# Optimization experiments

Measured on AMD Instinct MI355X. Metric: run time of the kernel, lower is better.

Reference implementation:

```python
import jax, jax.numpy as jnp
import numpy as np

NUM_STEPS = 8
THRESHOLD = 0.5


def _glorot(key, shape):
    fan_in = shape[0]
    return jax.random.normal(key, shape, dtype=jnp.float32) / np.sqrt(fan_in).astype(np.float32)


def setup_inputs() -> dict:
    key = jax.random.key(0)
    ks = jax.random.split(key, 24)
    B, APM = 2048, 32           # molecules, atoms per molecule
    N = B * APM                 # 65536 nodes
    E = N * 4                   # 262144 directed edges
    NF, EF, NH, EH, MA = 64, 16, 128, 128, 256
    inp = {}
    inp['mol_a_reprs'] = jax.random.normal(ks[0], (B, MA), dtype=jnp.float32)
    inp['node_features'] = jax.random.normal(ks[1], (N, NF), dtype=jnp.float32)
    inp['edge_features'] = jax.random.normal(ks[2], (E, EF), dtype=jnp.float32)
    inp['node_hidden0'] = jnp.zeros((N, NH), dtype=jnp.float32)
    inp['edge_hidden0'] = jnp.zeros((E, EH), dtype=jnp.float32)
    inp['edges'] = jax.random.randint(ks[3], (2, E), 0, N, dtype=jnp.int32)
    inp['batch_indices'] = jnp.repeat(jnp.arange(B, dtype=jnp.int32), APM)  # sorted, in-range
    # MPN weights (no bias)
    inp['W1'] = _glorot(ks[4], (NF, EH))   # src node features -> edge hidden
    inp['W2'] = _glorot(ks[5], (EF, EH))   # edge features -> edge hidden
    inp['W3'] = _glorot(ks[6], (NH, EH))   # src node hidden -> edge hidden
    inp['U1'] = _glorot(ks[7], (NF, NH))   # node features -> node hidden
    inp['U2'] = _glorot(ks[8], (EH, NH))   # aggregated edge hidden -> node hidden
    # pick-atom MLP: (MA+NH)->256->128->64->1
    inp['M1w'] = _glorot(ks[9], (MA + NH, 256)); inp['M1b'] = jnp.zeros((256,), jnp.float32)
    inp['M2w'] = _glorot(ks[10], (256, 128));    inp['M2b'] = jnp.zeros((128,), jnp.float32)
    inp['M3w'] = _glorot(ks[11], (128, 64));     inp['M3b'] = jnp.zeros((64,), jnp.float32)
    inp['M4w'] = _glorot(ks[12], (64, 1));       inp['M4b'] = jnp.zeros((1,), jnp.float32)
    return inp


def _mpn(node_features, edge_features, node_h, edge_h, src, dst, W1, W2, W3, U1, U2):
    N = node_features.shape[0]
    W1x_src = node_features[src] @ W1          # [E, EH], loop-invariant
    W2e = edge_features @ W2                   # [E, EH], loop-invariant
    U1x = node_features @ U1                   # [N, NH], loop-invariant
    for _ in range(NUM_STEPS):
        agg = jax.ops.segment_sum(edge_h, dst, num_segments=N)   # [N, EH]
        node_h = jax.nn.relu(U1x + agg @ U2)                     # [N, NH]
        edge_h = jax.nn.relu(W1x_src + W2e + node_h[src] @ W3)   # [E, EH]
    return node_h


def reference(mol_a_reprs, node_features, edge_features, node_hidden0, edge_hidden0,
              edges, batch_indices, W1, W2, W3, U1, U2,
              M1w, M1b, M2w, M2b, M3w, M3b, M4w, M4b):
    src, dst = edges[0], edges[1]
    node_h = _mpn(node_features, edge_features, node_hidden0, edge_hidden0,
                  src, dst, W1, W2, W3, U1, U2)
    b_atom_mol_a = mol_a_reprs[batch_indices]                    # index_select gather [N, MA]
    x = jnp.concatenate([node_h, b_atom_mol_a], axis=1)          # [N, NH+MA]
    x = jax.nn.relu(x @ M1w + M1b)
    x = jax.nn.relu(x @ M2w + M2b)
    x = jax.nn.relu(x @ M3w + M3b)
    p = jax.nn.sigmoid(x @ M4w + M4b)                            # [N, 1]
    return p >= THRESHOLD
```

## Files before the change

### kernel.cpp

```cpp
#include <hip/hip_runtime.h>
#include <cstddef>

#define NF 64
#define EF 16
#define NH 128
#define EH 128
#define MA 256

static inline int ceil_div(int a, int b) { return (a + b - 1) / b; }

__global__ __launch_bounds__(256) void gemm128_kernel(
    const float* __restrict__ A, const float* __restrict__ Bw,
    float* __restrict__ C,
    const float* __restrict__ addR, const int* __restrict__ addIdx,
    const float* __restrict__ bias, const int* __restrict__ gatherA,
    int M, int K, int Nc, int doRelu)
{
    __shared__ float As[16][132];
    __shared__ float Bs[16][132];
    const int tid = threadIdx.x;
    const int tx = tid & 15;
    const int ty = tid >> 4;
    const int m0 = blockIdx.y << 7;
    const int n0 = blockIdx.x << 7;

    const int lr = tid >> 1;
    const int lc = (tid & 1) << 3;
    const int br = tid >> 4;
    const int bc = (tid & 15) << 3;

    float acc[8][8];
#pragma unroll
    for (int i = 0; i < 8; ++i)
#pragma unroll
        for (int j = 0; j < 8; ++j) acc[i][j] = 0.0f;

    int arow = gatherA ? gatherA[m0 + lr] : (m0 + lr);
    const float* aptr = A + (size_t)arow * K + lc;

    for (int k0 = 0; k0 < K; k0 += 16) {
        float4 a0 = *(const float4*)(aptr + k0);
        float4 a1 = *(const float4*)(aptr + k0 + 4);
        float4 b0 = *(const float4*)(Bw + (size_t)(k0 + br) * Nc + n0 + bc);
        float4 b1 = *(const float4*)(Bw + (size_t)(k0 + br) * Nc + n0 + bc + 4);
        __syncthreads();
        As[lc + 0][lr] = a0.x; As[lc + 1][lr] = a0.y; As[lc + 2][lr] = a0.z; As[lc + 3][lr] = a0.w;
        As[lc + 4][lr] = a1.x; As[lc + 5][lr] = a1.y; As[lc + 6][lr] = a1.z; As[lc + 7][lr] = a1.w;
        *(float4*)&Bs[br][bc] = b0;
        *(float4*)&Bs[br][bc + 4] = b1;
        __syncthreads();
#pragma unroll
        for (int kk = 0; kk < 16; ++kk) {
            float4 av0 = *(const float4*)&As[kk][ty * 8];
            float4 av1 = *(const float4*)&As[kk][ty * 8 + 4];
            float4 bv0 = *(const float4*)&Bs[kk][tx * 8];
            float4 bv1 = *(const float4*)&Bs[kk][tx * 8 + 4];
            float a[8] = {av0.x, av0.y, av0.z, av0.w, av1.x, av1.y, av1.z, av1.w};
            float b[8] = {bv0.x, bv0.y, bv0.z, bv0.w, bv1.x, bv1.y, bv1.z, bv1.w};
#pragma unroll
            for (int i = 0; i < 8; ++i)
#pragma unroll
                for (int j = 0; j < 8; ++j)
                    acc[i][j] = fmaf(a[i], b[j], acc[i][j]);
        }
    }

    const int c = n0 + tx * 8;
    float4 bvl = make_float4(0.f, 0.f, 0.f, 0.f), bvh = bvl;
    if (bias) { bvl = *(const float4*)(bias + c); bvh = *(const float4*)(bias + c + 4); }
#pragma unroll
    for (int i = 0; i < 8; ++i) {
        int r = m0 + ty * 8 + i;
        float4 vl = make_float4(acc[i][0], acc[i][1], acc[i][2], acc[i][3]);
        float4 vh = make_float4(acc[i][4], acc[i][5], acc[i][6], acc[i][7]);
        if (addR) {
            int ar = addIdx ? addIdx[r] : r;
            float4 al = *(const float4*)(addR + (size_t)ar * Nc + c);
            float4 ah = *(const float4*)(addR + (size_t)ar * Nc + c + 4);
            vl.x += al.x; vl.y += al.y; vl.z += al.z; vl.w += al.w;
            vh.x += ah.x; vh.y += ah.y; vh.z += ah.z; vh.w += ah.w;
        }
        vl.x += bvl.x; vl.y += bvl.y; vl.z += bvl.z; vl.w += bvl.w;
        vh.x += bvh.x; vh.y += bvh.y; vh.z += bvh.z; vh.w += bvh.w;
        if (doRelu) {
            vl.x = fmaxf(vl.x, 0.f); vl.y = fmaxf(vl.y, 0.f); vl.z = fmaxf(vl.z, 0.f); vl.w = fmaxf(vl.w, 0.f);
            vh.x = fmaxf(vh.x, 0.f); vh.y = fmaxf(vh.y, 0.f); vh.z = fmaxf(vh.z, 0.f); vh.w = fmaxf(vh.w, 0.f);
        }
        *(float4*)(C + (size_t)r * Nc + c) = vl;
        *(float4*)(C + (size_t)r * Nc + c + 4) = vh;
    }
}

__global__ __launch_bounds__(256) void gemm_kernel(
    const float* __restrict__ A, const float* __restrict__ Bw,
    float* __restrict__ C,
    const float* __restrict__ addR, const int* __restrict__ addIdx,
    const float* __restrict__ bias,
    int M, int K, int Nc, int doRelu)
{
    __shared__ float As[16][64];
    __shared__ float Bs[16][64];
    const int tid = threadIdx.x;
    const int tx = tid & 15, ty = tid >> 4;
    const int m0 = blockIdx.y << 6;
    const int n0 = blockIdx.x << 6;
    const int lr = tid >> 2;
    const int lc = (tid & 3) << 2;
    const int bkr = tid >> 4;
    const int bc = (tid & 15) << 2;

    float acc[4][4];
#pragma unroll
    for (int i = 0; i < 4; ++i)
#pragma unroll
        for (int j = 0; j < 4; ++j) acc[i][j] = 0.0f;

    for (int k0 = 0; k0 < K; k0 += 16) {
        float4 a4 = *(const float4*)(A + (size_t)(m0 + lr) * K + (k0 + lc));
        float4 b4 = *(const float4*)(Bw + (size_t)(k0 + bkr) * Nc + (n0 + bc));
        __syncthreads();
        As[lc + 0][lr] = a4.x;
        As[lc + 1][lr] = a4.y;
        As[lc + 2][lr] = a4.z;
        As[lc + 3][lr] = a4.w;
        *(float4*)&Bs[bkr][bc] = b4;
        __syncthreads();
#pragma unroll
        for (int kk = 0; kk < 16; ++kk) {
            float a0 = As[kk][ty * 4 + 0];
            float a1 = As[kk][ty * 4 + 1];
            float a2 = As[kk][ty * 4 + 2];
            float a3 = As[kk][ty * 4 + 3];
            float b0 = Bs[kk][tx * 4 + 0];
            float b1 = Bs[kk][tx * 4 + 1];
            float b2 = Bs[kk][tx * 4 + 2];
            float b3 = Bs[kk][tx * 4 + 3];
            acc[0][0] += a0 * b0; acc[0][1] += a0 * b1; acc[0][2] += a0 * b2; acc[0][3] += a0 * b3;
            acc[1][0] += a1 * b0; acc[1][1] += a1 * b1; acc[1][2] += a1 * b2; acc[1][3] += a1 * b3;
            acc[2][0] += a2 * b0; acc[2][1] += a2 * b1; acc[2][2] += a2 * b2; acc[2][3] += a2 * b3;
            acc[3][0] += a3 * b0; acc[3][1] += a3 * b1; acc[3][2] += a3 * b2; acc[3][3] += a3 * b3;
        }
    }

    const int c = n0 + tx * 4;
    float4 bv = make_float4(0.f, 0.f, 0.f, 0.f);
    if (bias) bv = *(const float4*)(bias + c);
#pragma unroll
    for (int i = 0; i < 4; ++i) {
        int r = m0 + ty * 4 + i;
        float4 v = make_float4(acc[i][0], acc[i][1], acc[i][2], acc[i][3]);
        if (addR) {
            int ar = addIdx ? addIdx[r] : r;
            float4 ad = *(const float4*)(addR + (size_t)ar * Nc + c);
            v.x += ad.x; v.y += ad.y; v.z += ad.z; v.w += ad.w;
        }
        v.x += bv.x; v.y += bv.y; v.z += bv.z; v.w += bv.w;
        if (doRelu) {
            v.x = fmaxf(v.x, 0.f); v.y = fmaxf(v.y, 0.f);
            v.z = fmaxf(v.z, 0.f); v.w = fmaxf(v.w, 0.f);
        }
        *(float4*)(C + (size_t)r * Nc + c) = v;
    }
}

__global__ __launch_bounds__(256) void hist_kernel(const int* __restrict__ dst, int* __restrict__ deg, int E) {
    int e = blockIdx.x * 256 + threadIdx.x;
    if (e < E) atomicAdd(&deg[dst[e]], 1);
}

__global__ __launch_bounds__(256) void scan_block_kernel(const int* __restrict__ deg, int* __restrict__ rp,
                                                         int* __restrict__ bsum) {
    __shared__ int buf[256];
    int tid = threadIdx.x;
    int i = blockIdx.x * 256 + tid;
    int v = deg[i];
    buf[tid] = v;
    __syncthreads();
    for (int off = 1; off < 256; off <<= 1) {
        int t = (tid >= off) ? buf[tid - off] : 0;
        __syncthreads();
        buf[tid] += t;
        __syncthreads();
    }
    rp[i] = buf[tid] - v;
    if (tid == 255) bsum[blockIdx.x] = buf[255];
}

__global__ __launch_bounds__(256) void scan_top_kernel(const int* __restrict__ bsum, int* __restrict__ boff,
                                                       int* __restrict__ rp, int N) {
    __shared__ int buf[256];
    int tid = threadIdx.x;
    int v = bsum[tid];
    buf[tid] = v;
    __syncthreads();
    for (int off = 1; off < 256; off <<= 1) {
        int t = (tid >= off) ? buf[tid - off] : 0;
        __syncthreads();
        buf[tid] += t;
        __syncthreads();
    }
    boff[tid] = buf[tid] - v;
    if (tid == 255) rp[N] = buf[255];
}

__global__ __launch_bounds__(256) void scan_add_kernel(int* __restrict__ rp, int* __restrict__ cursor,
                                                       const int* __restrict__ boff) {
    int tid = threadIdx.x;
    int i = blockIdx.x * 256 + tid;
    int v = rp[i] + boff[blockIdx.x];
    rp[i] = v;
    cursor[i] = v;
}

__global__ __launch_bounds__(256) void scatter_kernel(const int* __restrict__ dst, const int* __restrict__ src,
                                                      int* __restrict__ cursor,
                                                      int* __restrict__ eid, int* __restrict__ srcS, int E) {
    int e = blockIdx.x * 256 + threadIdx.x;
    if (e < E) {
        int p = atomicAdd(&cursor[dst[e]], 1);
        eid[p] = e;
        srcS[p] = src[e];
    }
}

__global__ __launch_bounds__(256) void relu_copy_kernel(const float* __restrict__ in, float* __restrict__ out, int n4) {
    int i = blockIdx.x * 256 + threadIdx.x;
    if (i < n4) {
        float4 v = ((const float4*)in)[i];
        v.x = fmaxf(v.x, 0.f); v.y = fmaxf(v.y, 0.f);
        v.z = fmaxf(v.z, 0.f); v.w = fmaxf(v.w, 0.f);
        ((float4*)out)[i] = v;
    }
}

__global__ __launch_bounds__(128) void agg_kernel(const float* __restrict__ nodeT, const float* __restrict__ W2eS,
                                                  const int* __restrict__ rp, const int* __restrict__ srcS,
                                                  float* __restrict__ agg) {
    int n = blockIdx.x * 4 + threadIdx.y;
    int c = threadIdx.x << 2;
    int p0 = rp[n], p1 = rp[n + 1];
    float4 s = make_float4(0.f, 0.f, 0.f, 0.f);
    for (int p = p0; p < p1; ++p) {
        int sn = srcS[p];
        float4 t = *(const float4*)(nodeT + (size_t)sn * EH + c);
        float4 w = *(const float4*)(W2eS + (size_t)p * EH + c);
        s.x += fmaxf(t.x + w.x, 0.f);
        s.y += fmaxf(t.y + w.y, 0.f);
        s.z += fmaxf(t.z + w.z, 0.f);
        s.w += fmaxf(t.w + w.w, 0.f);
    }
    *(float4*)(agg + (size_t)n * EH + c) = s;
}

__global__ __launch_bounds__(256) void final_kernel(const float* __restrict__ x3, const float* __restrict__ w,
                                                    const float* __restrict__ b, int* __restrict__ out, int Nn) {
    int g = blockIdx.x * 256 + threadIdx.x;
    int n = g >> 6;
    int lane = threadIdx.x & 63;
    if (n < Nn) {
        float v = x3[(size_t)n * 64 + lane] * w[lane];
#pragma unroll
        for (int off = 32; off > 0; off >>= 1) v += __shfl_xor(v, off, 64);
        if (lane == 0) out[n] = (v + b[0]) >= 0.f ? 1 : 0;
    }
}

extern "C" void kernel_launch(void* const* d_in, const int* in_sizes, int n_in,
                              void* d_out, int out_size, void* d_ws, size_t ws_size,
                              hipStream_t stream)
{
    const float* mol_a = (const float*)d_in[0];
    const float* nf    = (const float*)d_in[1];
    const float* ef    = (const float*)d_in[2];
    const int*   edges = (const int*)d_in[5];
    const int*   batch = (const int*)d_in[6];
    const float* W1  = (const float*)d_in[7];
    const float* W2  = (const float*)d_in[8];
    const float* W3  = (const float*)d_in[9];
    const float* U1  = (const float*)d_in[10];
    const float* U2  = (const float*)d_in[11];
    const float* M1w = (const float*)d_in[12];
    const float* M1b = (const float*)d_in[13];
    const float* M2w = (const float*)d_in[14];
    const float* M2b = (const float*)d_in[15];
    const float* M3w = (const float*)d_in[16];
    const float* M3b = (const float*)d_in[17];
    const float* M4w = (const float*)d_in[18];
    const float* M4b = (const float*)d_in[19];

    const int N = in_sizes[3] / NH;
    const int E = in_sizes[4] / EH;
    const int B = in_sizes[0] / MA;
    const int* srcp = edges;
    const int* dstp = edges + E;

    char* ws = (char*)d_ws;
    size_t off = 0;
    auto alloc = [&](size_t bytes) -> char* {
        char* p = ws + off;
        off = (off + bytes + 255) & ~(size_t)255;
        return p;
    };
    int* deg     = (int*)alloc((size_t)N * 4);
    int* rp      = (int*)alloc(((size_t)N + 1) * 4);
    int* cursor  = (int*)alloc((size_t)N * 4);
    int* bsum    = (int*)alloc(256 * 4);
    int* boff    = (int*)alloc(256 * 4);
    int* eid     = (int*)alloc((size_t)E * 4);
    int* srcS    = (int*)alloc((size_t)E * 4);
    float* nodePre = (float*)alloc((size_t)N * EH * 4);
    float* U1x     = (float*)alloc((size_t)N * NH * 4);
    float* node_h  = (float*)alloc((size_t)N * NH * 4);
    float* nodeT   = (float*)alloc((size_t)N * EH * 4);
    float* aggp    = (float*)alloc((size_t)N * EH * 4);
    float* molPart = (float*)alloc((size_t)B * 256 * 4);
    float* W2eS    = (float*)alloc((size_t)E * EH * 4);
    float* x1 = (float*)W2eS;
    float* x2 = nodeT;
    float* x3 = aggp;

    hipMemsetAsync(deg, 0, (size_t)N * 4, stream);
    hist_kernel<<<ceil_div(E, 256), 256, 0, stream>>>(dstp, deg, E);
    scan_block_kernel<<<N / 256, 256, 0, stream>>>(deg, rp, bsum);
    scan_top_kernel<<<1, 256, 0, stream>>>(bsum, boff, rp, N);
    scan_add_kernel<<<N / 256, 256, 0, stream>>>(rp, cursor, boff);
    scatter_kernel<<<ceil_div(E, 256), 256, 0, stream>>>(dstp, srcp, cursor, eid, srcS, E);

    gemm128_kernel<<<dim3(1, N / 128), 256, 0, stream>>>(nf, W1, nodePre, nullptr, nullptr, nullptr, nullptr, N, NF, EH, 0);
    gemm128_kernel<<<dim3(1, E / 128), 256, 0, stream>>>(ef, W2, W2eS, nullptr, nullptr, nullptr, eid, E, EF, EH, 0);
    gemm128_kernel<<<dim3(1, N / 128), 256, 0, stream>>>(nf, U1, U1x, nullptr, nullptr, nullptr, nullptr, N, NF, NH, 0);

    relu_copy_kernel<<<(N * NH / 4) / 256, 256, 0, stream>>>(U1x, node_h, N * NH / 4);

    for (int s = 0; s < 7; ++s) {
        gemm128_kernel<<<dim3(1, N / 128), 256, 0, stream>>>(node_h, W3, nodeT, nodePre, nullptr, nullptr, nullptr, N, NH, EH, 0);
        agg_kernel<<<N / 4, dim3(32, 4), 0, stream>>>(nodeT, W2eS, rp, srcS, aggp);
        gemm128_kernel<<<dim3(1, N / 128), 256, 0, stream>>>(aggp, U2, node_h, U1x, nullptr, nullptr, nullptr, N, EH, NH, 1);
    }

    gemm_kernel<<<dim3(256 / 64, B / 64), 256, 0, stream>>>(mol_a, M1w + 128 * 256, molPart, nullptr, nullptr, M1b, B, MA, 256, 0);
    gemm128_kernel<<<dim3(2, N / 128), 256, 0, stream>>>(node_h, M1w, x1, molPart, batch, nullptr, nullptr, N, NH, 256, 1);
    gemm128_kernel<<<dim3(1, N / 128), 256, 0, stream>>>(x1, M2w, x2, nullptr, nullptr, M2b, nullptr, N, 256, 128, 1);
    gemm_kernel<<<dim3(1, N / 64), 256, 0, stream>>>(x2, M3w, x3, nullptr, nullptr, M3b, N, 128, 64, 1);
    final_kernel<<<ceil_div(N * 64, 256), 256, 0, stream>>>(x3, M4w, M4b, (int*)d_out, N);
}
```

Baseline: 1.387 ms.

## Double-buffer GEMM, fuse scan, relu copy, and final MLP layers

Replaces the tiled GEMM with a double-buffered shared-memory version that prefetches the next K tile while computing the current one. It also folds the initial relu copy into the first W3 GEMM's A load, merges the three-kernel scan into a single 1024-thread kernel, and fuses the M3 GEMM with the M4 dot product and threshold. The aggregation kernel now uses 8 rows per block. These changes cut kernel launches and intermediate traffic, at the cost of doubled LDS use per block and a serial single-block scan.

New measurement: 2.132 ms. 1.54x slower.

```diff
diff --git a/kernel.cpp b/kernel.cpp
--- a/kernel.cpp
+++ b/kernel.cpp
@@ -9,15 +9,15 @@
 
 static inline int ceil_div(int a, int b) { return (a + b - 1) / b; }
 
-__global__ __launch_bounds__(256) void gemm128_kernel(
+__global__ __launch_bounds__(256, 2) void gemm128_db(
     const float* __restrict__ A, const float* __restrict__ Bw,
     float* __restrict__ C,
     const float* __restrict__ addR, const int* __restrict__ addIdx,
     const float* __restrict__ bias, const int* __restrict__ gatherA,
-    int M, int K, int Nc, int doRelu)
+    int M, int K, int Nc, int doRelu, int reluA)
 {
-    __shared__ float As[16][132];
-    __shared__ float Bs[16][132];
+    __shared__ float As[2][16][132];
+    __shared__ float Bs[2][16][132];
     const int tid = threadIdx.x;
     const int tx = tid & 15;
     const int ty = tid >> 4;
@@ -37,33 +37,58 @@
 
     int arow = gatherA ? gatherA[m0 + lr] : (m0 + lr);
     const float* aptr = A + (size_t)arow * K + lc;
-
-    for (int k0 = 0; k0 < K; k0 += 16) {
-        float4 a0 = *(const float4*)(aptr + k0);
-        float4 a1 = *(const float4*)(aptr + k0 + 4);
-        float4 b0 = *(const float4*)(Bw + (size_t)(k0 + br) * Nc + n0 + bc);
-        float4 b1 = *(const float4*)(Bw + (size_t)(k0 + br) * Nc + n0 + bc + 4);
-        __syncthreads();
-        As[lc + 0][lr] = a0.x; As[lc + 1][lr] = a0.y; As[lc + 2][lr] = a0.z; As[lc + 3][lr] = a0.w;
-        As[lc + 4][lr] = a1.x; As[lc + 5][lr] = a1.y; As[lc + 6][lr] = a1.z; As[lc + 7][lr] = a1.w;
-        *(float4*)&Bs[br][bc] = b0;
-        *(float4*)&Bs[br][bc + 4] = b1;
-        __syncthreads();
-#pragma unroll
-        for (int kk = 0; kk < 16; ++kk) {
-            float4 av0 = *(const float4*)&As[kk][ty * 8];
-            float4 av1 = *(const float4*)&As[kk][ty * 8 + 4];
-            float4 bv0 = *(const float4*)&Bs[kk][tx * 8];
-            float4 bv1 = *(const float4*)&Bs[kk][tx * 8 + 4];
-            float a[8] = {av0.x, av0.y, av0.z, av0.w, av1.x, av1.y, av1.z, av1.w};
-            float b[8] = {bv0.x, bv0.y, bv0.z, bv0.w, bv1.x, bv1.y, bv1.z, bv1.w};
-#pragma unroll
-            for (int i = 0; i < 8; ++i)
-#pragma unroll
-                for (int j = 0; j < 8; ++j)
-                    acc[i][j] = fmaf(a[i], b[j], acc[i][j]);
+    const float* bptr = Bw + (size_t)br * Nc + n0 + bc;
+
+    float4 a0 = *(const float4*)(aptr);
+    float4 a1 = *(const float4*)(aptr + 4);
+    float4 b0 = *(const float4*)(bptr);
+    float4 b1 = *(const float4*)(bptr + 4);
+    if (reluA) {
+        a0.x = fmaxf(a0.x, 0.f); a0.y = fmaxf(a0.y, 0.f); a0.z = fmaxf(a0.z, 0.f); a0.w = fmaxf(a0.w, 0.f);
+        a1.x = fmaxf(a1.x, 0.f); a1.y = fmaxf(a1.y, 0.f); a1.z = fmaxf(a1.z, 0.f); a1.w = fmaxf(a1.w, 0.f);
+    }
+    As[0][lc + 0][lr] = a0.x; As[0][lc + 1][lr] = a0.y; As[0][lc + 2][lr] = a0.z; As[0][lc + 3][lr] = a0.w;
+    As[0][lc + 4][lr] = a1.x; As[0][lc + 5][lr] = a1.y; As[0][lc + 6][lr] = a1.z; As[0][lc + 7][lr] = a1.w;
+    *(float4*)&Bs[0][br][bc] = b0;
+    *(float4*)&Bs[0][br][bc + 4] = b1;
+    __syncthreads();
+
+#define GEMM_COMPUTE(BUF)                                                        \
+    _Pragma("unroll")                                                            \
+    for (int kk = 0; kk < 16; ++kk) {                                            \
+        float4 av0 = *(const float4*)&As[BUF][kk][ty * 8];                       \
+        float4 av1 = *(const float4*)&As[BUF][kk][ty * 8 + 4];                   \
+        float4 bv0 = *(const float4*)&Bs[BUF][kk][tx * 8];                       \
+        float4 bv1 = *(const float4*)&Bs[BUF][kk][tx * 8 + 4];                   \
+        float a[8] = {av0.x, av0.y, av0.z, av0.w, av1.x, av1.y, av1.z, av1.w};   \
+        float b[8] = {bv0.x, bv0.y, bv0.z, bv0.w, bv1.x, bv1.y, bv1.z, bv1.w};   \
+        _Pragma("unroll")                                                        \
+        for (int i = 0; i < 8; ++i)                                              \
+            _Pragma("unroll")                                                    \
+            for (int j = 0; j < 8; ++j)                                          \
+                acc[i][j] = fmaf(a[i], b[j], acc[i][j]);                         \
+    }
+
+    const int nt = K >> 4;
+    for (int t = 1; t < nt; ++t) {
+        float4 na0 = *(const float4*)(aptr + t * 16);
+        float4 na1 = *(const float4*)(aptr + t * 16 + 4);
+        float4 nb0 = *(const float4*)(bptr + (size_t)t * 16 * Nc);
+        float4 nb1 = *(const float4*)(bptr + (size_t)t * 16 * Nc + 4);
+        if (reluA) {
+            na0.x = fmaxf(na0.x, 0.f); na0.y = fmaxf(na0.y, 0.f); na0.z = fmaxf(na0.z, 0.f); na0.w = fmaxf(na0.w, 0.f);
+            na1.x = fmaxf(na1.x, 0.f); na1.y = fmaxf(na1.y, 0.f); na1.z = fmaxf(na1.z, 0.f); na1.w = fmaxf(na1.w, 0.f);
         }
-    }
+        const int cur = (t - 1) & 1, nxt = t & 1;
+        if (cur == 0) { GEMM_COMPUTE(0) } else { GEMM_COMPUTE(1) }
+        As[nxt][lc + 0][lr] = na0.x; As[nxt][lc + 1][lr] = na0.y; As[nxt][lc + 2][lr] = na0.z; As[nxt][lc + 3][lr] = na0.w;
+        As[nxt][lc + 4][lr] = na1.x; As[nxt][lc + 5][lr] = na1.y; As[nxt][lc + 6][lr] = na1.z; As[nxt][lc + 7][lr] = na1.w;
+        *(float4*)&Bs[nxt][br][bc] = nb0;
+        *(float4*)&Bs[nxt][br][bc + 4] = nb1;
+        __syncthreads();
+    }
+    if (((nt - 1) & 1) == 0) { GEMM_COMPUTE(0) } else { GEMM_COMPUTE(1) }
+#undef GEMM_COMPUTE
 
     const int c = n0 + tx * 8;
     float4 bvl = make_float4(0.f, 0.f, 0.f, 0.f), bvh = bvl;
@@ -91,125 +116,34 @@
     }
 }
 
-__global__ __launch_bounds__(256) void gemm_kernel(
-    const float* __restrict__ A, const float* __restrict__ Bw,
-    float* __restrict__ C,
-    const float* __restrict__ addR, const int* __restrict__ addIdx,
-    const float* __restrict__ bias,
-    int M, int K, int Nc, int doRelu)
-{
-    __shared__ float As[16][64];
-    __shared__ float Bs[16][64];
-    const int tid = threadIdx.x;
-    const int tx = tid & 15, ty = tid >> 4;
-    const int m0 = blockIdx.y << 6;
-    const int n0 = blockIdx.x << 6;
-    const int lr = tid >> 2;
-    const int lc = (tid & 3) << 2;
-    const int bkr = tid >> 4;
-    const int bc = (tid & 15) << 2;
-
-    float acc[4][4];
-#pragma unroll
-    for (int i = 0; i < 4; ++i)
-#pragma unroll
-        for (int j = 0; j < 4; ++j) acc[i][j] = 0.0f;
-
-    for (int k0 = 0; k0 < K; k0 += 16) {
-        float4 a4 = *(const float4*)(A + (size_t)(m0 + lr) * K + (k0 + lc));
-        float4 b4 = *(const float4*)(Bw + (size_t)(k0 + bkr) * Nc + (n0 + bc));
-        __syncthreads();
-        As[lc + 0][lr] = a4.x;
-        As[lc + 1][lr] = a4.y;
-        As[lc + 2][lr] = a4.z;
-        As[lc + 3][lr] = a4.w;
-        *(float4*)&Bs[bkr][bc] = b4;
-        __syncthreads();
-#pragma unroll
-        for (int kk = 0; kk < 16; ++kk) {
-            float a0 = As[kk][ty * 4 + 0];
-            float a1 = As[kk][ty * 4 + 1];
-            float a2 = As[kk][ty * 4 + 2];
-            float a3 = As[kk][ty * 4 + 3];
-            float b0 = Bs[kk][tx * 4 + 0];
-            float b1 = Bs[kk][tx * 4 + 1];
-            float b2 = Bs[kk][tx * 4 + 2];
-            float b3 = Bs[kk][tx * 4 + 3];
-            acc[0][0] += a0 * b0; acc[0][1] += a0 * b1; acc[0][2] += a0 * b2; acc[0][3] += a0 * b3;
-            acc[1][0] += a1 * b0; acc[1][1] += a1 * b1; acc[1][2] += a1 * b2; acc[1][3] += a1 * b3;
-            acc[2][0] += a2 * b0; acc[2][1] += a2 * b1; acc[2][2] += a2 * b2; acc[2][3] += a2 * b3;
-            acc[3][0] += a3 * b0; acc[3][1] += a3 * b1; acc[3][2] += a3 * b2; acc[3][3] += a3 * b3;
-        }
-    }
-
-    const int c = n0 + tx * 4;
-    float4 bv = make_float4(0.f, 0.f, 0.f, 0.f);
-    if (bias) bv = *(const float4*)(bias + c);
-#pragma unroll
-    for (int i = 0; i < 4; ++i) {
-        int r = m0 + ty * 4 + i;
-        float4 v = make_float4(acc[i][0], acc[i][1], acc[i][2], acc[i][3]);
-        if (addR) {
-            int ar = addIdx ? addIdx[r] : r;
-            float4 ad = *(const float4*)(addR + (size_t)ar * Nc + c);
-            v.x += ad.x; v.y += ad.y; v.z += ad.z; v.w += ad.w;
-        }
-        v.x += bv.x; v.y += bv.y; v.z += bv.z; v.w += bv.w;
-        if (doRelu) {
-            v.x = fmaxf(v.x, 0.f); v.y = fmaxf(v.y, 0.f);
-            v.z = fmaxf(v.z, 0.f); v.w = fmaxf(v.w, 0.f);
-        }
-        *(float4*)(C + (size_t)r * Nc + c) = v;
-    }
-}
-
 __global__ __launch_bounds__(256) void hist_kernel(const int* __restrict__ dst, int* __restrict__ deg, int E) {
     int e = blockIdx.x * 256 + threadIdx.x;
     if (e < E) atomicAdd(&deg[dst[e]], 1);
 }
 
-__global__ __launch_bounds__(256) void scan_block_kernel(const int* __restrict__ deg, int* __restrict__ rp,
-                                                         int* __restrict__ bsum) {
-    __shared__ int buf[256];
-    int tid = threadIdx.x;
-    int i = blockIdx.x * 256 + tid;
-    int v = deg[i];
-    buf[tid] = v;
+__global__ __launch_bounds__(1024) void scan_all_kernel(const int* __restrict__ deg, int* __restrict__ rp,
+                                                        int* __restrict__ cursor, int N) {
+    __shared__ int sums[1024];
+    const int tid = threadIdx.x;
+    const int per = N / 1024;
+    const int base = tid * per;
+    int tot = 0;
+    for (int i = 0; i < per; ++i) tot += deg[base + i];
+    sums[tid] = tot;
     __syncthreads();
-    for (int off = 1; off < 256; off <<= 1) {
-        int t = (tid >= off) ? buf[tid - off] : 0;
-        __syncthreads();
-        buf[tid] += t;
-        __syncthreads();
-    }
-    rp[i] = buf[tid] - v;
-    if (tid == 255) bsum[blockIdx.x] = buf[255];
-}
-
-__global__ __launch_bounds__(256) void scan_top_kernel(const int* __restrict__ bsum, int* __restrict__ boff,
-                                                       int* __restrict__ rp, int N) {
-    __shared__ int buf[256];
-    int tid = threadIdx.x;
-    int v = bsum[tid];
-    buf[tid] = v;
-    __syncthreads();
-    for (int off = 1; off < 256; off <<= 1) {
-        int t = (tid >= off) ? buf[tid - off] : 0;
-        __syncthreads();
-        buf[tid] += t;
-        __syncthreads();
-    }
-    boff[tid] = buf[tid] - v;
-    if (tid == 255) rp[N] = buf[255];
-}
-
-__global__ __launch_bounds__(256) void scan_add_kernel(int* __restrict__ rp, int* __restrict__ cursor,
-                                                       const int* __restrict__ boff) {
-    int tid = threadIdx.x;
-    int i = blockIdx.x * 256 + tid;
-    int v = rp[i] + boff[blockIdx.x];
-    rp[i] = v;
-    cursor[i] = v;
+    for (int off = 1; off < 1024; off <<= 1) {
+        int t = (tid >= off) ? sums[tid - off] : 0;
+        __syncthreads();
+        sums[tid] += t;
+        __syncthreads();
+    }
+    int prefix = sums[tid] - tot;
+    for (int i = 0; i < per; ++i) {
+        rp[base + i] = prefix;
+        cursor[base + i] = prefix;
+        prefix += deg[base + i];
+    }
+    if (tid == 1023) rp[N] = sums[1023];
 }
 
 __global__ __launch_bounds__(256) void scatter_kernel(const int* __restrict__ dst, const int* __restrict__ src,
@@ -223,20 +157,10 @@
     }
 }
 
-__global__ __launch_bounds__(256) void relu_copy_kernel(const float* __restrict__ in, float* __restrict__ out, int n4) {
-    int i = blockIdx.x * 256 + threadIdx.x;
-    if (i < n4) {
-        float4 v = ((const float4*)in)[i];
-        v.x = fmaxf(v.x, 0.f); v.y = fmaxf(v.y, 0.f);
-        v.z = fmaxf(v.z, 0.f); v.w = fmaxf(v.w, 0.f);
-        ((float4*)out)[i] = v;
-    }
-}
-
-__global__ __launch_bounds__(128) void agg_kernel(const float* __restrict__ nodeT, const float* __restrict__ W2eS,
+__global__ __launch_bounds__(256) void agg_kernel(const float* __restrict__ nodeT, const float* __restrict__ W2eS,
                                                   const int* __restrict__ rp, const int* __restrict__ srcS,
                                                   float* __restrict__ agg) {
-    int n = blockIdx.x * 4 + threadIdx.y;
+    int n = blockIdx.x * 8 + threadIdx.y;
     int c = threadIdx.x << 2;
     int p0 = rp[n], p1 = rp[n + 1];
     float4 s = make_float4(0.f, 0.f, 0.f, 0.f);
@@ -252,16 +176,67 @@
     *(float4*)(agg + (size_t)n * EH + c) = s;
 }
 
-__global__ __launch_bounds__(256) void final_kernel(const float* __restrict__ x3, const float* __restrict__ w,
-                                                    const float* __restrict__ b, int* __restrict__ out, int Nn) {
-    int g = blockIdx.x * 256 + threadIdx.x;
-    int n = g >> 6;
-    int lane = threadIdx.x & 63;
-    if (n < Nn) {
-        float v = x3[(size_t)n * 64 + lane] * w[lane];
-#pragma unroll
-        for (int off = 32; off > 0; off >>= 1) v += __shfl_xor(v, off, 64);
-        if (lane == 0) out[n] = (v + b[0]) >= 0.f ? 1 : 0;
+__global__ __launch_bounds__(256) void x3final_kernel(const float* __restrict__ x2, const float* __restrict__ M3w,
+                                                      const float* __restrict__ b3, const float* __restrict__ M4w,
+                                                      const float* __restrict__ b4, int* __restrict__ out) {
+    __shared__ float As[16][132];
+    __shared__ float Bs[16][68];
+    __shared__ float red[128][17];
+    const int tid = threadIdx.x;
+    const int tx = tid & 15;
+    const int ty = tid >> 4;
+    const int m0 = blockIdx.x << 7;
+    const int lr = tid >> 1, lc = (tid & 1) << 3;
+    const int br = tid >> 4, bc = (tid & 15) << 2;
+
+    float acc[8][4];
+#pragma unroll
+    for (int i = 0; i < 8; ++i)
+#pragma unroll
+        for (int j = 0; j < 4; ++j) acc[i][j] = 0.0f;
+
+    const float* aptr = x2 + (size_t)(m0 + lr) * 128 + lc;
+    for (int k0 = 0; k0 < 128; k0 += 16) {
+        float4 a0 = *(const float4*)(aptr + k0);
+        float4 a1 = *(const float4*)(aptr + k0 + 4);
+        float4 bv = *(const float4*)(M3w + (size_t)(k0 + br) * 64 + bc);
+        __syncthreads();
+        As[lc + 0][lr] = a0.x; As[lc + 1][lr] = a0.y; As[lc + 2][lr] = a0.z; As[lc + 3][lr] = a0.w;
+        As[lc + 4][lr] = a1.x; As[lc + 5][lr] = a1.y; As[lc + 6][lr] = a1.z; As[lc + 7][lr] = a1.w;
+        *(float4*)&Bs[br][bc] = bv;
+        __syncthreads();
+#pragma unroll
+        for (int kk = 0; kk < 16; ++kk) {
+            float4 av0 = *(const float4*)&As[kk][ty * 8];
+            float4 av1 = *(const float4*)&As[kk][ty * 8 + 4];
+            float4 bv0 = *(const float4*)&Bs[kk][tx * 4];
+            float a[8] = {av0.x, av0.y, av0.z, av0.w, av1.x, av1.y, av1.z, av1.w};
+            float b[4] = {bv0.x, bv0.y, bv0.z, bv0.w};
+#pragma unroll
+            for (int i = 0; i < 8; ++i)
+#pragma unroll
+                for (int j = 0; j < 4; ++j)
+                    acc[i][j] = fmaf(a[i], b[j], acc[i][j]);
+        }
+    }
+
+    const int c = tx * 4;
+    float4 b3v = *(const float4*)(b3 + c);
+    float4 w4v = *(const float4*)(M4w + c);
+#pragma unroll
+    for (int i = 0; i < 8; ++i) {
+        float p = fmaxf(acc[i][0] + b3v.x, 0.f) * w4v.x
+                + fmaxf(acc[i][1] + b3v.y, 0.f) * w4v.y
+                + fmaxf(acc[i][2] + b3v.z, 0.f) * w4v.z
+                + fmaxf(acc[i][3] + b3v.w, 0.f) * w4v.w;
+        red[ty * 8 + i][tx] = p;
+    }
+    __syncthreads();
+    if (tid < 128) {
+        float z = b4[0];
+#pragma unroll
+        for (int j = 0; j < 16; ++j) z += red[tid][j];
+        out[m0 + tid] = z >= 0.f ? 1 : 0;
     }
 }
 
@@ -304,8 +279,6 @@
     int* deg     = (int*)alloc((size_t)N * 4);
     int* rp      = (int*)alloc(((size_t)N + 1) * 4);
     int* cursor  = (int*)alloc((size_t)N * 4);
-    int* bsum    = (int*)alloc(256 * 4);
-    int* boff    = (int*)alloc(256 * 4);
     int* eid     = (int*)alloc((size_t)E * 4);
     int* srcS    = (int*)alloc((size_t)E * 4);
     float* nodePre = (float*)alloc((size_t)N * EH * 4);
@@ -317,30 +290,28 @@
     float* W2eS    = (float*)alloc((size_t)E * EH * 4);
     float* x1 = (float*)W2eS;
     float* x2 = nodeT;
-    float* x3 = aggp;
 
     hipMemsetAsync(deg, 0, (size_t)N * 4, stream);
     hist_kernel<<<ceil_div(E, 256), 256, 0, stream>>>(dstp, deg, E);
-    scan_block_kernel<<<N / 256, 256, 0, stream>>>(deg, rp, bsum);
-    scan_top_kernel<<<1, 256, 0, stream>>>(bsum, boff, rp, N);
-    scan_add_kernel<<<N / 256, 256, 0, stream>>>(rp, cursor, boff);
+    scan_all_kernel<<<1, 1024, 0, stream>>>(deg, rp, cursor, N);
     scatter_kernel<<<ceil_div(E, 256), 256, 0, stream>>>(dstp, srcp, cursor, eid, srcS, E);
 
-    gemm128_kernel<<<dim3(1, N / 128), 256, 0, stream>>>(nf, W1, nodePre, nullptr, nullptr, nullptr, nullptr, N, NF, EH, 0);
-    gemm128_kernel<<<dim3(1, E / 128), 256, 0, stream>>>(ef, W2, W2eS, nullptr, nullptr, nullptr, eid, E, EF, EH, 0);
-    gemm128_kernel<<<dim3(1, N / 128), 256, 0, stream>>>(nf, U1, U1x, nullptr, nullptr, nullptr, nullptr, N, NF, NH, 0);
-
-    relu_copy_kernel<<<(N * NH / 4) / 256, 256, 0, stream>>>(U1x, node_h, N * NH / 4);
-
-    for (int s = 0; s < 7; ++s) {
-        gemm128_kernel<<<dim3(1, N / 128), 256, 0, stream>>>(node_h, W3, nodeT, nodePre, nullptr, nullptr, nullptr, N, NH, EH, 0);
-        agg_kernel<<<N / 4, dim3(32, 4), 0, stream>>>(nodeT, W2eS, rp, srcS, aggp);
-        gemm128_kernel<<<dim3(1, N / 128), 256, 0, stream>>>(aggp, U2, node_h, U1x, nullptr, nullptr, nullptr, N, EH, NH, 1);
-    }
-
-    gemm_kernel<<<dim3(256 / 64, B / 64), 256, 0, stream>>>(mol_a, M1w + 128 * 256, molPart, nullptr, nullptr, M1b, B, MA, 256, 0);
-    gemm128_kernel<<<dim3(2, N / 128), 256, 0, stream>>>(node_h, M1w, x1, molPart, batch, nullptr, nullptr, N, NH, 256, 1);
-    gemm128_kernel<<<dim3(1, N / 128), 256, 0, stream>>>(x1, M2w, x2, nullptr, nullptr, M2b, nullptr, N, 256, 128, 1);
-    gemm_kernel<<<dim3(1, N / 64), 256, 0, stream>>>(x2, M3w, x3, nullptr, nullptr, M3b, N, 128, 64, 1);
-    final_kernel<<<ceil_div(N * 64, 256), 256, 0, stream>>>(x3, M4w, M4b, (int*)d_out, N);
-}
+    gemm128_db<<<dim3(1, N / 128), 256, 0, stream>>>(nf, W1, nodePre, nullptr, nullptr, nullptr, nullptr, N, NF, EH, 0, 0);
+    gemm128_db<<<dim3(1, E / 128), 256, 0, stream>>>(ef, W2, W2eS, nullptr, nullptr, nullptr, eid, E, EF, EH, 0, 0);
+    gemm128_db<<<dim3(1, N / 128), 256, 0, stream>>>(nf, U1, U1x, nullptr, nullptr, nullptr, nullptr, N, NF, NH, 0, 0);
+
+    gemm128_db<<<dim3(1, N / 128), 256, 0, stream>>>(U1x, W3, nodeT, nodePre, nullptr, nullptr, nullptr, N, NH, EH, 0, 1);
+
+    for (int s = 0; s < 6; ++s) {
+        agg_kernel<<<N / 8, dim3(32, 8), 0, stream>>>(nodeT, W2eS, rp, srcS, aggp);
+        gemm128_db<<<dim3(1, N / 128), 256, 0, stream>>>(aggp, U2, node_h, U1x, nullptr, nullptr, nullptr, N, EH, NH, 1, 0);
+        gemm128_db<<<dim3(1, N / 128), 256, 0, stream>>>(node_h, W3, nodeT, nodePre, nullptr, nullptr, nullptr, N, NH, EH, 0, 0);
+    }
+    agg_kernel<<<N / 8, dim3(32, 8), 0, stream>>>(nodeT, W2eS, rp, srcS, aggp);
+    gemm128_db<<<dim3(1, N / 128), 256, 0, stream>>>(aggp, U2, node_h, U1x, nullptr, nullptr, nullptr, N, EH, NH, 1, 0);
+
+    gemm128_db<<<dim3(2, B / 128), 256, 0, stream>>>(mol_a, M1w + 128 * 256, molPart, nullptr, nullptr, M1b, nullptr, B, MA, 256, 0, 0);
+    gemm128_db<<<dim3(2, N / 128), 256, 0, stream>>>(node_h, M1w, x1, molPart, batch, nullptr, nullptr, N, NH, 256, 1, 0);
+    gemm128_db<<<dim3(1, N / 128), 256, 0, stream>>>(x1, M2w, x2, nullptr, nullptr, M2b, nullptr, N, 256, 128, 1, 0);
+    x3final_kernel<<<N / 128, 256, 0, stream>>>(x2, M3w, M3b, M4w, M4b, (int*)d_out);
+}
```
